# Optimization experiments

Measured on AMD Instinct MI355X. Metric: run time of the kernel, lower is better.

The kernel has to match this reference:

```python
import jax, jax.numpy as jnp
import numpy as np

B, MAX_NPUS, MEM_SIZE = 16, 1024, 4096
IN_SIZE, REG_SIZE, MEM_DIM = 512, 256, 128
GRU_IN = IN_SIZE + MEM_DIM
MMU_OUT = MEM_DIM * 5 + 4  # 644


def setup_inputs() -> dict:
    key = jax.random.key(0)
    ks = jax.random.split(key, 12)
    s = 0.02
    return {
        "input_vector": jax.random.normal(ks[0], (B, IN_SIZE), jnp.float32),
        "registers": jax.random.normal(ks[1], (B, MAX_NPUS, REG_SIZE), jnp.float32),
        "memory_context": jax.random.normal(ks[2], (B, MEM_SIZE, MEM_DIM), jnp.float32),
        "W_ih": jax.random.normal(ks[3], (3 * REG_SIZE, GRU_IN), jnp.float32) * s,
        "b_ih": jax.random.normal(ks[4], (3 * REG_SIZE,), jnp.float32) * s,
        "W_hh": jax.random.normal(ks[5], (3 * REG_SIZE, REG_SIZE), jnp.float32) * s,
        "b_hh": jax.random.normal(ks[6], (3 * REG_SIZE,), jnp.float32) * s,
        "W_mmu": jax.random.normal(ks[7], (MMU_OUT, REG_SIZE), jnp.float32) * s,
        "b_mmu": jax.random.normal(ks[8], (MMU_OUT,), jnp.float32) * s,
        "W_out": jax.random.normal(ks[9], (IN_SIZE, REG_SIZE), jnp.float32) * s,
        "b_out": jax.random.normal(ks[10], (IN_SIZE,), jnp.float32) * s,
        "active_npus": MAX_NPUS,
    }


def reference(input_vector, registers, memory_context, W_ih, b_ih, W_hh, b_hh,
              W_mmu, b_mmu, W_out, b_out, active_npus):
    md, rs = MEM_DIM, REG_SIZE
    curr = registers[:, :active_npus, :]                      # [B,N,rs]
    mmu = jnp.einsum('bnr,or->bno', curr, W_mmu) + b_mmu      # [B,N,5*md+4]
    query = mmu[..., :md]
    w_key = mmu[..., md:2 * md]
    w_val = mmu[..., 2 * md:3 * md]
    w_gate = jax.nn.sigmoid(mmu[..., 3 * md:3 * md + 1])
    ssd_key = mmu[..., 3 * md + 1:4 * md + 1]
    ssd_val = mmu[..., 4 * md + 1:5 * md + 1]
    ssd_gate = jax.nn.softmax(mmu[..., 5 * md + 1:5 * md + 4], axis=-1)
    # attention read over shared memory
    scores = jnp.einsum('bnd,bmd->bnm', query, memory_context) / jnp.sqrt(jnp.float32(md))
    attn = jax.nn.softmax(scores, axis=-1)                    # [B,N,M]
    read_data = jnp.einsum('bnm,bmd->bnd', attn, memory_context)
    # GRU cell (torch GRUCell semantics, gate order r,z,n)
    inp = jnp.broadcast_to(input_vector[:, None, :], (curr.shape[0], active_npus, input_vector.shape[-1]))
    x = jnp.concatenate([inp, read_data], axis=-1)            # [B,N,in+md]
    gi = jnp.einsum('bni,oi->bno', x, W_ih) + b_ih            # [B,N,3*rs]
    gh = jnp.einsum('bnr,or->bno', curr, W_hh) + b_hh
    gi_r, gi_z, gi_n = gi[..., :rs], gi[..., rs:2 * rs], gi[..., 2 * rs:]
    gh_r, gh_z, gh_n = gh[..., :rs], gh[..., rs:2 * rs], gh[..., 2 * rs:]
    r = jax.nn.sigmoid(gi_r + gh_r)
    z = jax.nn.sigmoid(gi_z + gh_z)
    n = jnp.tanh(gi_n + r * gh_n)
    new_regs = (1.0 - z) * n + z * curr                       # [B,N,rs]
    output_active = jnp.einsum('bnr,or->bno', new_regs, W_out) + b_out
    return (output_active, new_regs, w_key, w_val, w_gate, ssd_key, ssd_val, ssd_gate)
```

## Files before the change

kernel.cpp:

```cpp
#include <hip/hip_runtime.h>
#include <hip/hip_bf16.h>
#include <math.h>

#define B_      16
#define NPUS    1024
#define MEMS    4096
#define INS     512
#define RS      256
#define MD      128
#define GRUIN   640
#define MMUO    644
#define NROWS   (B_*NPUS)

#define O_OUT   0u
#define O_REGS  8388608u
#define O_WKEY  12582912u
#define O_WVAL  14680064u
#define O_WGATE 16777216u
#define O_SSDK  16793600u
#define O_SSDV  18890752u
#define O_SSDG  20987904u

typedef __attribute__((ext_vector_type(8))) short bf16x8;
typedef __attribute__((ext_vector_type(4))) float f32x4;
typedef __attribute__((ext_vector_type(4))) unsigned short u16x4;

__device__ __forceinline__ float sigf(float x){ return 1.f/(1.f+__expf(-x)); }
__device__ __forceinline__ unsigned short bfu(float x){
    __hip_bfloat16 h = __float2bfloat16(x);
    return __builtin_bit_cast(unsigned short, h);
}
__device__ __forceinline__ float b2f(unsigned short u){
    unsigned v = ((unsigned)u) << 16;
    return __builtin_bit_cast(float, v);
}
__device__ __forceinline__ void gload16(const void* g, void* s)
{
    __builtin_amdgcn_global_load_lds(
        (const __attribute__((address_space(1))) void*)g,
        (__attribute__((address_space(3))) void*)s, 16, 0, 0);
}

__global__ __launch_bounds__(256) void k_cvt(const float* __restrict__ src,
                                             unsigned short* __restrict__ dst, int n4)
{
    int i = blockIdx.x*256 + threadIdx.x;
    if (i >= n4) return;
    float4 v = ((const float4*)src)[i];
    u16x4 o = { bfu(v.x), bfu(v.y), bfu(v.z), bfu(v.w) };
    ((u16x4*)dst)[i] = o;
}

__global__ __launch_bounds__(256) void k_cvt5(const float* __restrict__ s0, unsigned short* __restrict__ d0,
                                              const float* __restrict__ s1, unsigned short* __restrict__ d1,
                                              const float* __restrict__ s2, unsigned short* __restrict__ d2,
                                              const float* __restrict__ s3, unsigned short* __restrict__ d3,
                                              const float* __restrict__ s4, unsigned short* __restrict__ d4)
{
    int gi = blockIdx.x*256 + threadIdx.x;
    const float* s; unsigned short* d; int idx;
    if      (gi < 41216)  { s = s0; d = d0; idx = gi; }
    else if (gi < 164096) { s = s1; d = d1; idx = gi - 41216; }
    else if (gi < 213248) { s = s2; d = d2; idx = gi - 164096; }
    else if (gi < 246016) { s = s3; d = d3; idx = gi - 213248; }
    else                  { s = s4; d = d4; idx = gi - 246016; }
    float4 v = ((const float4*)s)[idx];
    u16x4 o = { bfu(v.x), bfu(v.y), bfu(v.z), bfu(v.w) };
    ((u16x4*)d)[idx] = o;
}

__global__ __launch_bounds__(256) void k_gi(const float* __restrict__ inp,
                                            const float* __restrict__ Wih,
                                            float* __restrict__ gi0)
{
    __shared__ float xs[INS];
    const int b = blockIdx.x, seg = blockIdx.y;
    const int t = threadIdx.x;
    for (int i = t; i < INS; i += 256) xs[i] = inp[(size_t)b*INS + i];
    __syncthreads();
    const int o = seg*256 + t;
    const float* wrow = Wih + (size_t)o*GRUIN;
    float a0 = 0.f, a1 = 0.f, a2 = 0.f, a3 = 0.f;
    for (int k = 0; k < INS; k += 4) {
        float4 wv = *(const float4*)(wrow + k);
        a0 += xs[k]*wv.x; a1 += xs[k+1]*wv.y; a2 += xs[k+2]*wv.z; a3 += xs[k+3]*wv.w;
    }
    gi0[(size_t)b*768 + o] = (a0 + a1) + (a2 + a3);
}

__global__ __launch_bounds__(256) void k_conv(const float* __restrict__ mem,
                                              __hip_bfloat16* __restrict__ memB,
                                              __hip_bfloat16* __restrict__ memT)
{
    __shared__ float Ms[32][129];
    const int t = threadIdx.x;
    const int b = blockIdx.x >> 7;
    const int m0 = (blockIdx.x & 127) << 5;
    const float* src = mem + ((size_t)b*MEMS + m0)*MD;
    for (int idx = t; idx < 32*128; idx += 256) {
        int m = idx >> 7, d = idx & 127;
        float v = src[(size_t)m*MD + d];
        Ms[m][d] = v;
        memB[((size_t)b*MEMS + m0 + m)*MD + d] = __float2bfloat16(v);
    }
    __syncthreads();
    for (int idx = t; idx < 128*32; idx += 256) {
        int d = idx >> 5, m = idx & 31;
        memT[((size_t)b*MD + d)*MEMS + m0 + m] = __float2bfloat16(Ms[m][d]);
    }
}

__global__ __launch_bounds__(256) void k_mmu(const __hip_bfloat16* __restrict__ Ab,
                                             const __hip_bfloat16* __restrict__ Wb,
                                             const float* __restrict__ bias,
                                             float* __restrict__ out,
                                             __hip_bfloat16* __restrict__ qbf)
{
    __shared__ __hip_bfloat16 At[2][64][32];
    __shared__ __hip_bfloat16 Bt[2][256][32];
    const int t = threadIdx.x, w = t >> 6, l = t & 63;
    const int lg = l >> 4, ll = l & 15;
    const int m0 = blockIdx.x*64;
    const int n0 = blockIdx.y*256;
    f32x4 acc[16];
    #pragma unroll
    for (int c = 0; c < 16; c++) acc[c] = (f32x4){0,0,0,0};

    const char* aSrc;
    {
        int row = t >> 2, cc = t & 3;
        int gc = cc ^ ((row >> 1) & 3);
        aSrc = (const char*)((const short*)Ab + (size_t)(m0+row)*RS) + gc*16;
    }
    const char* bSrc[4];
    #pragma unroll
    for (int j = 0; j < 4; j++) {
        int ci = j*256 + t;
        int row = ci >> 2, cc = ci & 3;
        int gc = cc ^ ((row >> 1) & 3);
        bSrc[j] = (const char*)((const short*)Wb + (size_t)(n0+row)*RS) + gc*16;
    }

    auto stage2 = [&](int buf, int it) {
        int off = it*64;
        char* abase = (char*)(&At[buf][0][0]) + (size_t)(w << 6)*16;
        gload16(aSrc + off, abase);
        #pragma unroll
        for (int j = 0; j < 4; j++) {
            char* bbase = (char*)(&Bt[buf][0][0]) + (size_t)(j*256 + (w << 6))*16;
            gload16(bSrc[j] + off, bbase);
        }
    };

    stage2(0, 0);
    asm volatile("s_waitcnt vmcnt(0)" ::: "memory");
    __syncthreads();
    int cur = 0;
    const int arow = (w << 4) + ll;
    const int aswz = ((lg ^ ((arow >> 1) & 3)) << 4);
    for (int it = 0; it < 8; ++it) {
        if (it + 1 < 8) stage2(cur ^ 1, it + 1);
        const char* ab = (const char*)(&At[cur][0][0]);
        const char* bb = (const char*)(&Bt[cur][0][0]);
        bf16x8 af = *(const bf16x8*)(ab + arow*64 + aswz);
        #pragma unroll
        for (int c = 0; c < 16; c++) {
            int r0 = c*16 + ll;
            int sw = ((lg ^ ((r0 >> 1) & 3)) << 4);
            bf16x8 bf = *(const bf16x8*)(bb + (size_t)r0*64 + sw);
            acc[c] = __builtin_amdgcn_mfma_f32_16x16x32_bf16(af, bf, acc[c], 0, 0, 0);
        }
        asm volatile("s_waitcnt vmcnt(0)" ::: "memory");
        __syncthreads();
        cur ^= 1;
    }
    const int wm0 = m0 + (w << 4);
    #pragma unroll
    for (int c = 0; c < 16; c++) {
        int o = n0 + c*16 + ll;
        if (o >= MMUO) continue;
        float bv = bias[o];
        #pragma unroll
        for (int r = 0; r < 4; r++) {
            int row = wm0 + lg*4 + r;
            float v = acc[c][r] + bv;
            if      (o < MD)        qbf[(size_t)row*MD + o] = __float2bfloat16(v * 0.08838834764831845f);
            else if (o < 2*MD)      out[O_WKEY + (size_t)row*MD + (o -   MD)] = v;
            else if (o < 3*MD)      out[O_WVAL + (size_t)row*MD + (o - 2*MD)] = v;
            else if (o == 3*MD)     out[O_WGATE + row] = sigf(v);
            else if (o < 4*MD + 1)  out[O_SSDK + (size_t)row*MD + (o - (3*MD+1))] = v;
            else if (o < 5*MD + 1)  out[O_SSDV + (size_t)row*MD + (o - (4*MD+1))] = v;
            else                    out[O_SSDG + (size_t)row*3  + (o - (5*MD+1))] = v;
        }
    }
}

__global__ void k_softmax3(float* __restrict__ out)
{
    int r = blockIdx.x*256 + threadIdx.x;
    if (r >= NROWS) return;
    float* p = out + O_SSDG + (size_t)r*3;
    float a = p[0], b = p[1], c = p[2];
    float m = fmaxf(a, fmaxf(b, c));
    float ea = __expf(a-m), eb = __expf(b-m), ec = __expf(c-m);
    float inv = 1.f/(ea+eb+ec);
    p[0] = ea*inv; p[1] = eb*inv; p[2] = ec*inv;
}

__global__ __launch_bounds__(256, 4) void k_attn(const __hip_bfloat16* __restrict__ qb,
                                                 const __hip_bfloat16* __restrict__ memB,
                                                 const __hip_bfloat16* __restrict__ memT,
                                                 unsigned short* __restrict__ Opart,
                                                 float* __restrict__ MLpart)
{
    __shared__ __hip_bfloat16 Kt[2][32][128];
    __shared__ __hip_bfloat16 Vt[2][128][32];
    __shared__ __hip_bfloat16 Pl[4][16][40];
    const int t = threadIdx.x, w = t >> 6, l = t & 63;
    const int lg = l >> 4, ll = l & 15;
    const int bid = blockIdx.x;
    const int xcd = bid & 7, rest = bid >> 3;
    const int b = xcd + ((rest >> 6) << 3);
    const int sub = rest & 63;
    const int qblk = sub >> 2, kh = sub & 3;
    const int qrow0 = (b << 10) + (qblk << 6) + (w << 4);
    const int k_beg = kh << 10;
    const float THR = 4.0f;

    const short* Q = (const short*)qb;
    bf16x8 qf[4];
    #pragma unroll
    for (int ks = 0; ks < 4; ks++)
        qf[ks] = *(const bf16x8*)(Q + (size_t)(qrow0 + ll)*MD + ks*32 + lg*8);

    f32x4 O[8];
    #pragma unroll
    for (int dt = 0; dt < 8; dt++) O[dt] = (f32x4){0.f,0.f,0.f,0.f};
    float m_run[4], lsum[4];
    #pragma unroll
    for (int r = 0; r < 4; r++) { m_run[r] = -INFINITY; lsum[r] = 0.f; }

    const char* MbB = (const char*)memB + (size_t)b*MEMS*MD*2;
    const char* MtB = (const char*)memT + (size_t)b*MD*MEMS*2;

    auto stage = [&](int buf, int it) {
        const int k0 = k_beg + it*32;
        char* kbase = (char*)(&Kt[buf][0][0]);
        char* vbase = (char*)(&Vt[buf][0][0]);
        #pragma unroll
        for (int j = 0; j < 2; j++) {
            int ci = (w << 7) + (j << 6) + l;
            int krow = ci >> 4, cc = ci & 15;
            int gc = cc ^ (krow & 7);
            gload16(MbB + (size_t)(k0 + krow)*256 + gc*16,
                    kbase + (size_t)((w << 7) + (j << 6))*16);
        }
        #pragma unroll
        for (int j = 0; j < 2; j++) {
            int ci = (w << 7) + (j << 6) + l;
            int drow = ci >> 2, cc = ci & 3;
            int gc = cc ^ ((drow >> 1) & 3);
            gload16(MtB + (size_t)drow*(MEMS*2) + (size_t)k0*2 + gc*16,
                    vbase + (size_t)((w << 7) + (j << 6))*16);
        }
    };

    stage(0, 0);
    asm volatile("s_waitcnt vmcnt(0)" ::: "memory");
    asm volatile("s_barrier" ::: "memory");
    int cur = 0;
    const int NIT = 1024/32;
    const int vsw = ((lg ^ ((ll >> 1) & 3)) << 4);
    for (int it = 0; it < NIT; ++it) {
        if (it + 1 < NIT) {
            stage(cur ^ 1, it + 1);
            asm volatile("s_waitcnt vmcnt(4)" ::: "memory");
        } else {
            asm volatile("s_waitcnt vmcnt(0)" ::: "memory");
        }
        asm volatile("s_barrier" ::: "memory");
        const char* kbase = (const char*)(&Kt[cur][0][0]);
        const char* vbase = (const char*)(&Vt[cur][0][0]);
        f32x4 s0 = (f32x4){0,0,0,0}, s1 = (f32x4){0,0,0,0};
        #pragma unroll
        for (int ks = 0; ks < 4; ks++) {
            int c0 = ks*4 + lg;
            int sw = (c0 ^ (ll & 7)) << 4;
            bf16x8 kf0 = *(const bf16x8*)(kbase + (size_t)ll*256 + sw);
            bf16x8 kf1 = *(const bf16x8*)(kbase + (size_t)(16 + ll)*256 + sw);
            s0 = __builtin_amdgcn_mfma_f32_16x16x32_bf16(qf[ks], kf0, s0, 0, 0, 0);
            s1 = __builtin_amdgcn_mfma_f32_16x16x32_bf16(qf[ks], kf1, s1, 0, 0, 0);
        }
        bool need = false;
        #pragma unroll
        for (int r = 0; r < 4; r++) {
            need |= (s0[r] > m_run[r] + THR);
            need |= (s1[r] > m_run[r] + THR);
        }
        if (__any(need)) {
            #pragma unroll
            for (int r = 0; r < 4; r++) {
                float v = fmaxf(s0[r], s1[r]);
                v = fmaxf(v, __shfl_xor(v, 1));
                v = fmaxf(v, __shfl_xor(v, 2));
                v = fmaxf(v, __shfl_xor(v, 4));
                v = fmaxf(v, __shfl_xor(v, 8));
                float mnew = fmaxf(m_run[r], v);
                float alpha = __expf(m_run[r] - mnew);
                m_run[r] = mnew;
                lsum[r] *= alpha;
                #pragma unroll
                for (int dt = 0; dt < 8; dt++) O[dt][r] *= alpha;
            }
        }
        #pragma unroll
        for (int r = 0; r < 4; r++) {
            float p0 = __expf(s0[r] - m_run[r]);
            float p1 = __expf(s1[r] - m_run[r]);
            Pl[w][lg*4 + r][ll]      = __float2bfloat16(p0);
            Pl[w][lg*4 + r][16 + ll] = __float2bfloat16(p1);
            lsum[r] += p0 + p1;
        }
        __builtin_amdgcn_wave_barrier();
        bf16x8 pa = *(const bf16x8*)(&Pl[w][ll][lg*8]);
        __builtin_amdgcn_wave_barrier();
        #pragma unroll
        for (int dt = 0; dt < 8; dt++) {
            bf16x8 vf = *(const bf16x8*)(vbase + (size_t)(dt*16 + ll)*64 + vsw);
            O[dt] = __builtin_amdgcn_mfma_f32_16x16x32_bf16(pa, vf, O[dt], 0, 0, 0);
        }
        asm volatile("s_barrier" ::: "memory");
        cur ^= 1;
    }
    #pragma unroll
    for (int r = 0; r < 4; r++) {
        float s = lsum[r];
        s += __shfl_xor(s, 1);
        s += __shfl_xor(s, 2);
        s += __shfl_xor(s, 4);
        s += __shfl_xor(s, 8);
        lsum[r] = s;
    }
    #pragma unroll
    for (int dt = 0; dt < 8; dt++)
        #pragma unroll
        for (int r = 0; r < 4; r++) {
            int row = qrow0 + lg*4 + r;
            Opart[((size_t)row*4 + kh)*128 + dt*16 + ll] = bfu(O[dt][r]);
        }
    if (ll == 0) {
        #pragma unroll
        for (int r = 0; r < 4; r++) {
            int row = qrow0 + lg*4 + r;
            MLpart[((size_t)row*4 + kh)*2 + 0] = m_run[r];
            MLpart[((size_t)row*4 + kh)*2 + 1] = lsum[r];
        }
    }
}

__global__ __launch_bounds__(256) void k_comb(const unsigned short* __restrict__ Opart,
                                              const float* __restrict__ MLpart,
                                              __hip_bfloat16* __restrict__ rdb)
{
    const int t = threadIdx.x;
    const int row = blockIdx.x*64 + (t >> 2);
    const int c0 = (t & 3) * 32;
    float m[4], lv[4], a[4];
    float M = -INFINITY;
    #pragma unroll
    for (int i = 0; i < 4; i++) {
        m[i]  = MLpart[((size_t)row*4 + i)*2 + 0];
        lv[i] = MLpart[((size_t)row*4 + i)*2 + 1];
        M = fmaxf(M, m[i]);
    }
    float L = 0.f;
    #pragma unroll
    for (int i = 0; i < 4; i++) { a[i] = __expf(m[i] - M); L += a[i]*lv[i]; }
    float invL = 1.f / L;
    #pragma unroll
    for (int i = 0; i < 4; i++) a[i] *= invL;
    unsigned short* dst = (unsigned short*)rdb + (size_t)row*128 + c0;
    #pragma unroll
    for (int j = 0; j < 8; j++) {
        float acc0=0.f, acc1=0.f, acc2=0.f, acc3=0.f;
        #pragma unroll
        for (int i = 0; i < 4; i++) {
            u16x4 x = ((const u16x4*)(Opart + ((size_t)row*4 + i)*128 + c0))[j];
            acc0 += a[i]*b2f(x[0]); acc1 += a[i]*b2f(x[1]);
            acc2 += a[i]*b2f(x[2]); acc3 += a[i]*b2f(x[3]);
        }
        u16x4 o = { bfu(acc0), bfu(acc1), bfu(acc2), bfu(acc3) };
        ((u16x4*)dst)[j] = o;
    }
}

__global__ __launch_bounds__(256) void k_gru(const float* __restrict__ gi0,
                                             const __hip_bfloat16* __restrict__ rdb,
                                             const __hip_bfloat16* __restrict__ regsb,
                                             const float* __restrict__ regs,
                                             const __hip_bfloat16* __restrict__ Wihb,
                                             const float* __restrict__ bih,
                                             const __hip_bfloat16* __restrict__ Whhb,
                                             const float* __restrict__ bhh,
                                             float* __restrict__ newregs,
                                             __hip_bfloat16* __restrict__ nregsb)
{
    __shared__ __hip_bfloat16 At[2][64][32];
    __shared__ __hip_bfloat16 Bt[2][192][32];
    const int t = threadIdx.x, w = t >> 6, l = t & 63;
    const int lg = l >> 4, ll = l & 15;
    const int m0 = blockIdx.x*64;
    const int n0 = blockIdx.y*64;
    const int batch = blockIdx.x >> 4;
    const short* Rd = (const short*)rdb;
    const short* Hb = (const short*)regsb;
    const short* Wi = (const short*)Wihb;
    const short* Wh = (const short*)Whhb;

    f32x4 aR[4], aZ[4], aNi[4], aNh[4];
    #pragma unroll
    for (int c = 0; c < 4; c++) {
        int o = n0 + c*16 + ll;
        float gR = gi0[(size_t)batch*768 + o];
        float gZ = gi0[(size_t)batch*768 + 256 + o];
        float gN = gi0[(size_t)batch*768 + 512 + o];
        aR[c]  = (f32x4){gR,gR,gR,gR};
        aZ[c]  = (f32x4){gZ,gZ,gZ,gZ};
        aNi[c] = (f32x4){gN,gN,gN,gN};
        aNh[c] = (f32x4){0,0,0,0};
    }

    const int aci = (w << 6) + l;
    const int arow_s = aci >> 2, acc_s = aci & 3;
    const int agc = acc_s ^ ((arow_s >> 1) & 3);
    const char* aSrcA = (const char*)(Rd + (size_t)(m0+arow_s)*MD) + agc*16;
    const char* aSrcB = (const char*)(Hb + (size_t)(m0+arow_s)*RS) + agc*16;
    const char* bSrcA0; const char* bSrcA1; const char* bSrcA2;
    const char* bSrcB0; const char* bSrcB1; const char* bSrcB2;
    {
        int ci, row, cc, gc, g, col;
        ci = w*192 + 0*64 + l; row = ci >> 2; cc = ci & 3; gc = cc ^ ((row >> 1) & 3);
        g = row >> 6; col = row & 63;
        bSrcA0 = (const char*)(Wi + (size_t)(g*RS + n0 + col)*GRUIN + INS) + gc*16;
        bSrcB0 = (const char*)(Wh + (size_t)(g*RS + n0 + col)*RS) + gc*16;
        ci = w*192 + 1*64 + l; row = ci >> 2; cc = ci & 3; gc = cc ^ ((row >> 1) & 3);
        g = row >> 6; col = row & 63;
        bSrcA1 = (const char*)(Wi + (size_t)(g*RS + n0 + col)*GRUIN + INS) + gc*16;
        bSrcB1 = (const char*)(Wh + (size_t)(g*RS + n0 + col)*RS) + gc*16;
        ci = w*192 + 2*64 + l; row = ci >> 2; cc = ci & 3; gc = cc ^ ((row >> 1) & 3);
        g = row >> 6; col = row & 63;
        bSrcA2 = (const char*)(Wi + (size_t)(g*RS + n0 + col)*GRUIN + INS) + gc*16;
        bSrcB2 = (const char*)(Wh + (size_t)(g*RS + n0 + col)*RS) + gc*16;
    }

    const int NITA = 4, NIT = 12;
    auto stage = [&](int buf, int it) {
        char* abase = (char*)(&At[buf][0][0]) + (size_t)(w << 6)*16;
        char* bbase = (char*)(&Bt[buf][0][0]) + (size_t)(w*192)*16;
        const char *as, *b0, *b1, *b2;
        if (it < NITA) {
            int off = it*64;
            as = aSrcA + off; b0 = bSrcA0 + off; b1 = bSrcA1 + off; b2 = bSrcA2 + off;
        } else {
            int off = (it - NITA)*64;
            as = aSrcB + off; b0 = bSrcB0 + off; b1 = bSrcB1 + off; b2 = bSrcB2 + off;
        }
        gload16(as, abase);
        gload16(b0, bbase);
        gload16(b1, bbase + 64*16);
        gload16(b2, bbase + 128*16);
    };

    stage(0, 0);
    asm volatile("s_waitcnt vmcnt(0)" ::: "memory");
    __syncthreads();
    int cur = 0;
    const int arow = (w << 4) + ll;
    const int aswz = ((lg ^ ((arow >> 1) & 3)) << 4);
    for (int it = 0; it < NIT; ++it) {
        if (it + 1 < NIT) stage(cur ^ 1, it + 1);
        const char* ab = (const char*)(&At[cur][0][0]);
        const char* bb = (const char*)(&Bt[cur][0][0]);
        bf16x8 af = *(const bf16x8*)(ab + arow*64 + aswz);
        if (it < NITA) {
            #pragma unroll
            for (int c = 0; c < 4; c++) {
                int r0 = c*16 + ll;
                int sw = ((lg ^ ((r0 >> 1) & 3)) << 4);
                bf16x8 bR = *(const bf16x8*)(bb + (size_t)r0*64 + sw);
                bf16x8 bZ = *(const bf16x8*)(bb + (size_t)(r0 + 64)*64 + sw);
                bf16x8 bN = *(const bf16x8*)(bb + (size_t)(r0 + 128)*64 + sw);
                aR[c]  = __builtin_amdgcn_mfma_f32_16x16x32_bf16(af, bR, aR[c],  0, 0, 0);
                aZ[c]  = __builtin_amdgcn_mfma_f32_16x16x32_bf16(af, bZ, aZ[c],  0, 0, 0);
                aNi[c] = __builtin_amdgcn_mfma_f32_16x16x32_bf16(af, bN, aNi[c], 0, 0, 0);
            }
        } else {
            #pragma unroll
            for (int c = 0; c < 4; c++) {
                int r0 = c*16 + ll;
                int sw = ((lg ^ ((r0 >> 1) & 3)) << 4);
                bf16x8 bR = *(const bf16x8*)(bb + (size_t)r0*64 + sw);
                bf16x8 bZ = *(const bf16x8*)(bb + (size_t)(r0 + 64)*64 + sw);
                bf16x8 bN = *(const bf16x8*)(bb + (size_t)(r0 + 128)*64 + sw);
                aR[c]  = __builtin_amdgcn_mfma_f32_16x16x32_bf16(af, bR, aR[c],  0, 0, 0);
                aZ[c]  = __builtin_amdgcn_mfma_f32_16x16x32_bf16(af, bZ, aZ[c],  0, 0, 0);
                aNh[c] = __builtin_amdgcn_mfma_f32_16x16x32_bf16(af, bN, aNh[c], 0, 0, 0);
            }
        }
        asm volatile("s_waitcnt vmcnt(0)" ::: "memory");
        __syncthreads();
        cur ^= 1;
    }
    const int wm0 = m0 + (w << 4);
    #pragma unroll
    for (int c = 0; c < 4; c++) {
        int o = n0 + c*16 + ll;
        float bR = bih[o]        + bhh[o];
        float bZ = bih[o +   RS] + bhh[o +   RS];
        float bNi = bih[o + 2*RS];
        float bNh = bhh[o + 2*RS];
        #pragma unroll
        for (int r = 0; r < 4; r++) {
            int row = wm0 + lg*4 + r;
            float rr = sigf(aR[c][r] + bR);
            float zz = sigf(aZ[c][r] + bZ);
            float nn = tanhf(aNi[c][r] + bNi + rr*(aNh[c][r] + bNh));
            float cv = regs[(size_t)row*RS + o];
            float nv = (1.f - zz)*nn + zz*cv;
            newregs[(size_t)row*RS + o] = nv;
            nregsb[(size_t)row*RS + o] = __float2bfloat16(nv);
        }
    }
}

__global__ __launch_bounds__(256) void k_out(const __hip_bfloat16* __restrict__ Ab,
                                             const __hip_bfloat16* __restrict__ Wb,
                                             const float* __restrict__ bias,
                                             float* __restrict__ out0)
{
    __shared__ __hip_bfloat16 At[2][64][32];
    __shared__ __hip_bfloat16 Bt[2][256][32];
    const int t = threadIdx.x, w = t >> 6, l = t & 63;
    const int lg = l >> 4, ll = l & 15;
    const int m0 = blockIdx.x*64;
    const int n0 = blockIdx.y*256;
    f32x4 acc[16];
    #pragma unroll
    for (int c = 0; c < 16; c++) acc[c] = (f32x4){0,0,0,0};

    const char* aSrc;
    {
        int row = t >> 2, cc = t & 3;
        int gc = cc ^ ((row >> 1) & 3);
        aSrc = (const char*)((const short*)Ab + (size_t)(m0+row)*RS) + gc*16;
    }
    const char* bSrc[4];
    #pragma unroll
    for (int j = 0; j < 4; j++) {
        int ci = j*256 + t;
        int row = ci >> 2, cc = ci & 3;
        int gc = cc ^ ((row >> 1) & 3);
        bSrc[j] = (const char*)((const short*)Wb + (size_t)(n0+row)*RS) + gc*16;
    }

    auto stage = [&](int buf, int it) {
        int off = it*64;
        char* abase = (char*)(&At[buf][0][0]) + (size_t)(w << 6)*16;
        gload16(aSrc + off, abase);
        #pragma unroll
        for (int j = 0; j < 4; j++) {
            char* bbase = (char*)(&Bt[buf][0][0]) + (size_t)(j*256 + (w << 6))*16;
            gload16(bSrc[j] + off, bbase);
        }
    };

    stage(0, 0);
    asm volatile("s_waitcnt vmcnt(0)" ::: "memory");
    __syncthreads();
    int cur = 0;
    const int arow = (w << 4) + ll;
    const int aswz = ((lg ^ ((arow >> 1) & 3)) << 4);
    for (int it = 0; it < 8; ++it) {
        if (it + 1 < 8) stage(cur ^ 1, it + 1);
        const char* ab = (const char*)(&At[cur][0][0]);
        const char* bb = (const char*)(&Bt[cur][0][0]);
        bf16x8 af = *(const bf16x8*)(ab + arow*64 + aswz);
        #pragma unroll
        for (int c = 0; c < 16; c++) {
            int r0 = c*16 + ll;
            int sw = ((lg ^ ((r0 >> 1) & 3)) << 4);
            bf16x8 bf = *(const bf16x8*)(bb + (size_t)r0*64 + sw);
            acc[c] = __builtin_amdgcn_mfma_f32_16x16x32_bf16(af, bf, acc[c], 0, 0, 0);
        }
        asm volatile("s_waitcnt vmcnt(0)" ::: "memory");
        __syncthreads();
        cur ^= 1;
    }
    const int wm0 = m0 + (w << 4);
    #pragma unroll
    for (int c = 0; c < 16; c++) {
        int o = n0 + c*16 + ll;
        float bv = bias[o];
        #pragma unroll
        for (int r = 0; r < 4; r++) {
            int row = wm0 + lg*4 + r;
            out0[(size_t)row*INS + o] = acc[c][r] + bv;
        }
    }
}

extern "C" void kernel_launch(void* const* d_in, const int* in_sizes, int n_in,
                              void* d_out, int out_size, void* d_ws, size_t ws_size,
                              hipStream_t stream)
{
    const float* inp  = (const float*)d_in[0];
    const float* regs = (const float*)d_in[1];
    const float* mem  = (const float*)d_in[2];
    const float* Wih  = (const float*)d_in[3];
    const float* bih  = (const float*)d_in[4];
    const float* Whh  = (const float*)d_in[5];
    const float* bhh  = (const float*)d_in[6];
    const float* Wmmu = (const float*)d_in[7];
    const float* bmmu = (const float*)d_in[8];
    const float* Wout = (const float*)d_in[9];
    const float* bout = (const float*)d_in[10];
    float* out = (float*)d_out;

    char* ws = (char*)d_ws;
    __hip_bfloat16* qbf    = (__hip_bfloat16*)(ws);
    __hip_bfloat16* rdb    = (__hip_bfloat16*)(ws + ((size_t)4<<20));
    __hip_bfloat16* memB   = (__hip_bfloat16*)(ws + ((size_t)8<<20));
    __hip_bfloat16* memT   = (__hip_bfloat16*)(ws + ((size_t)24<<20));
    __hip_bfloat16* regsb  = (__hip_bfloat16*)(ws + ((size_t)40<<20));
    __hip_bfloat16* nregsb = (__hip_bfloat16*)(ws + ((size_t)48<<20));
    __hip_bfloat16* Wmmub  = (__hip_bfloat16*)(ws + ((size_t)56<<20));
    __hip_bfloat16* Wihb   = (__hip_bfloat16*)(ws + ((size_t)56<<20) + ( 1<<20));
    __hip_bfloat16* Whhb   = (__hip_bfloat16*)(ws + ((size_t)56<<20) + ( 2<<20));
    __hip_bfloat16* Woutb  = (__hip_bfloat16*)(ws + ((size_t)56<<20) + ( 3<<20));
    __hip_bfloat16* inpb   = (__hip_bfloat16*)(ws + ((size_t)56<<20) + ( 4<<20));
    float*          MLpart = (float*)(ws + ((size_t)61<<20));
    float*          gi0    = (float*)(ws + ((size_t)61<<20) + (1<<19));
    unsigned short* Opart  = (unsigned short*)(out + O_OUT);

    dim3 ggi(B_, 3);
    k_gi<<<ggi, 256, 0, stream>>>(inp, Wih, gi0);
    k_cvt5<<<969, 256, 0, stream>>>(Wmmu, (unsigned short*)Wmmub,
                                    Wih,  (unsigned short*)Wihb,
                                    Whh,  (unsigned short*)Whhb,
                                    Wout, (unsigned short*)Woutb,
                                    inp,  (unsigned short*)inpb);
    k_cvt<<<(4194304/4 + 255)/256, 256, 0, stream>>>(regs, (unsigned short*)regsb, 4194304/4);
    k_conv<<<B_*128, 256, 0, stream>>>(mem, memB, memT);

    dim3 g1(NROWS/64, 3);
    k_mmu<<<g1, 256, 0, stream>>>(regsb, Wmmub, bmmu, out, qbf);
    k_softmax3<<<NROWS/256, 256, 0, stream>>>(out);
    k_attn<<<1024, 256, 0, stream>>>(qbf, memB, memT, Opart, MLpart);
    k_comb<<<NROWS/64, 256, 0, stream>>>(Opart, MLpart, rdb);
    dim3 g3(NROWS/64, 4);
    k_gru<<<g3, 256, 0, stream>>>(gi0, rdb, regsb, regs, Wihb, bih, Whhb, bhh,
                                  out + O_REGS, nregsb);
    dim3 g4(NROWS/64, 2);
    k_out<<<g4, 256, 0, stream>>>(nregsb, Woutb, bout, out);
}
```

Before: 172.9 us.

## Halve N-tile in MMU/out GEMMs and fuse 3-way softmax into MMU epilogue

Shrinks the N tile of k_mmu and k_out from 256 to 128 columns, doubling the grid and cutting LDS and accumulator registers, and adds occupancy hints (launch_bounds 256,4) to k_mmu, k_gru and k_out. The ssd_gate softmax is now computed in the k_mmu epilogue with lane shuffles, which removes the separate k_softmax3 launch and its extra pass over that output. In exchange the A tile is loaded more times across the larger grid, the last N block (640..767) does mostly padded work, and the shuffle-based softmax depends on the accumulator lane layout.

```diff
diff --git a/kernel.cpp b/kernel.cpp
--- a/kernel.cpp
+++ b/kernel.cpp
@@ -110,21 +110,21 @@
     }
 }
 
-__global__ __launch_bounds__(256) void k_mmu(const __hip_bfloat16* __restrict__ Ab,
-                                             const __hip_bfloat16* __restrict__ Wb,
-                                             const float* __restrict__ bias,
-                                             float* __restrict__ out,
-                                             __hip_bfloat16* __restrict__ qbf)
+__global__ __launch_bounds__(256, 4) void k_mmu(const __hip_bfloat16* __restrict__ Ab,
+                                                const __hip_bfloat16* __restrict__ Wb,
+                                                const float* __restrict__ bias,
+                                                float* __restrict__ out,
+                                                __hip_bfloat16* __restrict__ qbf)
 {
     __shared__ __hip_bfloat16 At[2][64][32];
-    __shared__ __hip_bfloat16 Bt[2][256][32];
+    __shared__ __hip_bfloat16 Bt[2][128][32];
     const int t = threadIdx.x, w = t >> 6, l = t & 63;
     const int lg = l >> 4, ll = l & 15;
     const int m0 = blockIdx.x*64;
-    const int n0 = blockIdx.y*256;
-    f32x4 acc[16];
-    #pragma unroll
-    for (int c = 0; c < 16; c++) acc[c] = (f32x4){0,0,0,0};
+    const int n0 = blockIdx.y*128;
+    f32x4 acc[8];
+    #pragma unroll
+    for (int c = 0; c < 8; c++) acc[c] = (f32x4){0,0,0,0};
 
     const char* aSrc;
     {
@@ -132,39 +132,39 @@
         int gc = cc ^ ((row >> 1) & 3);
         aSrc = (const char*)((const short*)Ab + (size_t)(m0+row)*RS) + gc*16;
     }
-    const char* bSrc[4];
-    #pragma unroll
-    for (int j = 0; j < 4; j++) {
-        int ci = j*256 + t;
+    const char* bSrc[2];
+    #pragma unroll
+    for (int j = 0; j < 2; j++) {
+        int ci = w*128 + j*64 + l;
         int row = ci >> 2, cc = ci & 3;
         int gc = cc ^ ((row >> 1) & 3);
         bSrc[j] = (const char*)((const short*)Wb + (size_t)(n0+row)*RS) + gc*16;
     }
 
-    auto stage2 = [&](int buf, int it) {
+    auto stage = [&](int buf, int it) {
         int off = it*64;
         char* abase = (char*)(&At[buf][0][0]) + (size_t)(w << 6)*16;
         gload16(aSrc + off, abase);
         #pragma unroll
-        for (int j = 0; j < 4; j++) {
-            char* bbase = (char*)(&Bt[buf][0][0]) + (size_t)(j*256 + (w << 6))*16;
+        for (int j = 0; j < 2; j++) {
+            char* bbase = (char*)(&Bt[buf][0][0]) + (size_t)(w*128 + j*64)*16;
             gload16(bSrc[j] + off, bbase);
         }
     };
 
-    stage2(0, 0);
+    stage(0, 0);
     asm volatile("s_waitcnt vmcnt(0)" ::: "memory");
     __syncthreads();
     int cur = 0;
     const int arow = (w << 4) + ll;
     const int aswz = ((lg ^ ((arow >> 1) & 3)) << 4);
     for (int it = 0; it < 8; ++it) {
-        if (it + 1 < 8) stage2(cur ^ 1, it + 1);
+        if (it + 1 < 8) stage(cur ^ 1, it + 1);
         const char* ab = (const char*)(&At[cur][0][0]);
         const char* bb = (const char*)(&Bt[cur][0][0]);
         bf16x8 af = *(const bf16x8*)(ab + arow*64 + aswz);
         #pragma unroll
-        for (int c = 0; c < 16; c++) {
+        for (int c = 0; c < 8; c++) {
             int r0 = c*16 + ll;
             int sw = ((lg ^ ((r0 >> 1) & 3)) << 4);
             bf16x8 bf = *(const bf16x8*)(bb + (size_t)r0*64 + sw);
@@ -176,9 +176,9 @@
     }
     const int wm0 = m0 + (w << 4);
     #pragma unroll
-    for (int c = 0; c < 16; c++) {
+    for (int c = 0; c < 8; c++) {
         int o = n0 + c*16 + ll;
-        if (o >= MMUO) continue;
+        if (o > 640) continue;
         float bv = bias[o];
         #pragma unroll
         for (int r = 0; r < 4; r++) {
@@ -189,22 +189,26 @@
             else if (o < 3*MD)      out[O_WVAL + (size_t)row*MD + (o - 2*MD)] = v;
             else if (o == 3*MD)     out[O_WGATE + row] = sigf(v);
             else if (o < 4*MD + 1)  out[O_SSDK + (size_t)row*MD + (o - (3*MD+1))] = v;
-            else if (o < 5*MD + 1)  out[O_SSDV + (size_t)row*MD + (o - (4*MD+1))] = v;
-            else                    out[O_SSDG + (size_t)row*3  + (o - (5*MD+1))] = v;
-        }
-    }
-}
-
-__global__ void k_softmax3(float* __restrict__ out)
-{
-    int r = blockIdx.x*256 + threadIdx.x;
-    if (r >= NROWS) return;
-    float* p = out + O_SSDG + (size_t)r*3;
-    float a = p[0], b = p[1], c = p[2];
-    float m = fmaxf(a, fmaxf(b, c));
-    float ea = __expf(a-m), eb = __expf(b-m), ec = __expf(c-m);
-    float inv = 1.f/(ea+eb+ec);
-    p[0] = ea*inv; p[1] = eb*inv; p[2] = ec*inv;
+            else                    out[O_SSDV + (size_t)row*MD + (o - (4*MD+1))] = v;
+        }
+    }
+    if (n0 == 640) {
+        #pragma unroll
+        for (int r = 0; r < 4; r++) {
+            int o = n0 + ll;
+            float vr = acc[0][r] + ((o < MMUO) ? bias[o] : 0.f);
+            float va = __shfl(vr, lg*16 + 1);
+            float vb = __shfl(vr, lg*16 + 2);
+            float vc = __shfl(vr, lg*16 + 3);
+            float mm = fmaxf(va, fmaxf(vb, vc));
+            float ea = __expf(va-mm), eb = __expf(vb-mm), ec = __expf(vc-mm);
+            float inv = 1.f/(ea+eb+ec);
+            int row = wm0 + lg*4 + r;
+            if (ll == 1) out[O_SSDG + (size_t)row*3 + 0] = ea*inv;
+            if (ll == 2) out[O_SSDG + (size_t)row*3 + 1] = eb*inv;
+            if (ll == 3) out[O_SSDG + (size_t)row*3 + 2] = ec*inv;
+        }
+    }
 }
 
 __global__ __launch_bounds__(256, 4) void k_attn(const __hip_bfloat16* __restrict__ qb,
@@ -394,16 +398,16 @@
     }
 }
 
-__global__ __launch_bounds__(256) void k_gru(const float* __restrict__ gi0,
-                                             const __hip_bfloat16* __restrict__ rdb,
-                                             const __hip_bfloat16* __restrict__ regsb,
-                                             const float* __restrict__ regs,
-                                             const __hip_bfloat16* __restrict__ Wihb,
-                                             const float* __restrict__ bih,
-                                             const __hip_bfloat16* __restrict__ Whhb,
-                                             const float* __restrict__ bhh,
-                                             float* __restrict__ newregs,
-                                             __hip_bfloat16* __restrict__ nregsb)
+__global__ __launch_bounds__(256, 4) void k_gru(const float* __restrict__ gi0,
+                                                const __hip_bfloat16* __restrict__ rdb,
+                                                const __hip_bfloat16* __restrict__ regsb,
+                                                const float* __restrict__ regs,
+                                                const __hip_bfloat16* __restrict__ Wihb,
+                                                const float* __restrict__ bih,
+                                                const __hip_bfloat16* __restrict__ Whhb,
+                                                const float* __restrict__ bhh,
+                                                float* __restrict__ newregs,
+                                                __hip_bfloat16* __restrict__ nregsb)
 {
     __shared__ __hip_bfloat16 At[2][64][32];
     __shared__ __hip_bfloat16 Bt[2][192][32];
@@ -533,20 +537,20 @@
     }
 }
 
-__global__ __launch_bounds__(256) void k_out(const __hip_bfloat16* __restrict__ Ab,
-                                             const __hip_bfloat16* __restrict__ Wb,
-                                             const float* __restrict__ bias,
-                                             float* __restrict__ out0)
+__global__ __launch_bounds__(256, 4) void k_out(const __hip_bfloat16* __restrict__ Ab,
+                                                const __hip_bfloat16* __restrict__ Wb,
+                                                const float* __restrict__ bias,
+                                                float* __restrict__ out0)
 {
     __shared__ __hip_bfloat16 At[2][64][32];
-    __shared__ __hip_bfloat16 Bt[2][256][32];
+    __shared__ __hip_bfloat16 Bt[2][128][32];
     const int t = threadIdx.x, w = t >> 6, l = t & 63;
     const int lg = l >> 4, ll = l & 15;
     const int m0 = blockIdx.x*64;
-    const int n0 = blockIdx.y*256;
-    f32x4 acc[16];
-    #pragma unroll
-    for (int c = 0; c < 16; c++) acc[c] = (f32x4){0,0,0,0};
+    const int n0 = blockIdx.y*128;
+    f32x4 acc[8];
+    #pragma unroll
+    for (int c = 0; c < 8; c++) acc[c] = (f32x4){0,0,0,0};
 
     const char* aSrc;
     {
@@ -554,10 +558,10 @@
         int gc = cc ^ ((row >> 1) & 3);
         aSrc = (const char*)((const short*)Ab + (size_t)(m0+row)*RS) + gc*16;
     }
-    const char* bSrc[4];
-    #pragma unroll
-    for (int j = 0; j < 4; j++) {
-        int ci = j*256 + t;
+    const char* bSrc[2];
+    #pragma unroll
+    for (int j = 0; j < 2; j++) {
+        int ci = w*128 + j*64 + l;
         int row = ci >> 2, cc = ci & 3;
         int gc = cc ^ ((row >> 1) & 3);
         bSrc[j] = (const char*)((const short*)Wb + (size_t)(n0+row)*RS) + gc*16;
@@ -568,8 +572,8 @@
         char* abase = (char*)(&At[buf][0][0]) + (size_t)(w << 6)*16;
         gload16(aSrc + off, abase);
         #pragma unroll
-        for (int j = 0; j < 4; j++) {
-            char* bbase = (char*)(&Bt[buf][0][0]) + (size_t)(j*256 + (w << 6))*16;
+        for (int j = 0; j < 2; j++) {
+            char* bbase = (char*)(&Bt[buf][0][0]) + (size_t)(w*128 + j*64)*16;
             gload16(bSrc[j] + off, bbase);
         }
     };
@@ -586,7 +590,7 @@
         const char* bb = (const char*)(&Bt[cur][0][0]);
         bf16x8 af = *(const bf16x8*)(ab + arow*64 + aswz);
         #pragma unroll
-        for (int c = 0; c < 16; c++) {
+        for (int c = 0; c < 8; c++) {
             int r0 = c*16 + ll;
             int sw = ((lg ^ ((r0 >> 1) & 3)) << 4);
             bf16x8 bf = *(const bf16x8*)(bb + (size_t)r0*64 + sw);
@@ -598,7 +602,7 @@
     }
     const int wm0 = m0 + (w << 4);
     #pragma unroll
-    for (int c = 0; c < 16; c++) {
+    for (int c = 0; c < 8; c++) {
         int o = n0 + c*16 + ll;
         float bv = bias[o];
         #pragma unroll
@@ -652,14 +656,13 @@
     k_cvt<<<(4194304/4 + 255)/256, 256, 0, stream>>>(regs, (unsigned short*)regsb, 4194304/4);
     k_conv<<<B_*128, 256, 0, stream>>>(mem, memB, memT);
 
-    dim3 g1(NROWS/64, 3);
+    dim3 g1(NROWS/64, 6);
     k_mmu<<<g1, 256, 0, stream>>>(regsb, Wmmub, bmmu, out, qbf);
-    k_softmax3<<<NROWS/256, 256, 0, stream>>>(out);
     k_attn<<<1024, 256, 0, stream>>>(qbf, memB, memT, Opart, MLpart);
     k_comb<<<NROWS/64, 256, 0, stream>>>(Opart, MLpart, rdb);
     dim3 g3(NROWS/64, 4);
     k_gru<<<g3, 256, 0, stream>>>(gi0, rdb, regsb, regs, Wihb, bih, Whhb, bhh,
                                   out + O_REGS, nregsb);
-    dim3 g4(NROWS/64, 2);
+    dim3 g4(NROWS/64, 4);
     k_out<<<g4, 256, 0, stream>>>(nregsb, Woutb, bout, out);
 }
```

Result: faster. 158.0 us (-8.6%).
